# Kernel optimization log

Hardware: AMD Instinct MI355X
Metric: run time of the kernel (lower is better)

## Reference

```python
import jax, jax.numpy as jnp
import numpy as np

NQ = 9  # 9 qubits per 3x3 patch; state shape (M, 2,...,2), axis (NQ-q) holds qubit q (qiskit little-endian)

def _ax(q):
    return NQ - q

def _bcast(theta):
    theta = jnp.asarray(theta)
    if theta.ndim == 1:  # per-patch angle -> broadcast over 8 remaining qubit axes
        return theta.reshape((-1,) + (1,) * (NQ - 1))
    return theta

def apply_1q(state, q, m00, m01, m10, m11):
    ax = _ax(q)
    s0 = jnp.take(state, 0, axis=ax)
    s1 = jnp.take(state, 1, axis=ax)
    return jnp.stack([m00 * s0 + m01 * s1, m10 * s0 + m11 * s1], axis=ax)

def apply_ry(state, q, theta):
    th = _bcast(theta) * 0.5
    c = jnp.cos(th).astype(state.dtype)
    s = jnp.sin(th).astype(state.dtype)
    return apply_1q(state, q, c, -s, s, c)

def apply_rz(state, q, theta):
    th = _bcast(theta) * 0.5
    e = jnp.exp(-1j * th.astype(jnp.complex64))
    return apply_1q(state, q, e, 0.0, 0.0, jnp.conj(e))

def apply_cx(state, c, t):
    axc, axt = _ax(c), _ax(t)
    sc0 = jnp.take(state, 0, axis=axc)
    sc1 = jnp.take(state, 1, axis=axc)
    axt2 = axt - 1 if axt > axc else axt
    sc1 = jnp.flip(sc1, axis=axt2)  # X on target within control=1 subspace
    return jnp.stack([sc0, sc1], axis=axc)

def apply_crx(state, c, t, theta):
    axc, axt = _ax(c), _ax(t)
    sc0 = jnp.take(state, 0, axis=axc)
    sc1 = jnp.take(state, 1, axis=axc)
    axt2 = axt - 1 if axt > axc else axt
    t0 = jnp.take(sc1, 0, axis=axt2)
    t1 = jnp.take(sc1, 1, axis=axt2)
    co = jnp.cos(theta * 0.5)
    si = jnp.sin(theta * 0.5)
    sc1 = jnp.stack([co * t0 - 1j * si * t1, -1j * si * t0 + co * t1], axis=axt2)
    return jnp.stack([sc0, sc1], axis=axc)

def qcnn_batched(angles, w):
    """angles: (M, 9) input rotation angles. w: (42,) shared weights. Returns (M, 3) = [<X>,<Y>,<Z>] on qubit 0."""
    M = angles.shape[0]
    state = jnp.zeros((M,) + (2,) * NQ, dtype=jnp.complex64)
    state = state.at[(slice(None),) + (0,) * NQ].set(1.0)
    for q in range(NQ):  # input encoding
        state = apply_ry(state, q, angles[:, q])
    wi = 0
    # conv1: RY + RZ on all 9 qubits, ring CNOT
    for q in range(NQ):
        state = apply_ry(state, q, w[wi]); wi += 1
    for q in range(NQ):
        state = apply_rz(state, q, w[wi]); wi += 1
    for i in range(NQ):
        state = apply_cx(state, i, (i + 1) % NQ)
    # pool1: 6 CRX gates
    for (c, t) in [(1, 0), (2, 0), (4, 3), (5, 3), (7, 6), (8, 6)]:
        state = apply_crx(state, c, t, w[wi]); wi += 1
    # conv2 on qubits [0,3,6]
    for q in [0, 3, 6]:
        state = apply_ry(state, q, w[wi]); wi += 1
    for q in [0, 3, 6]:
        state = apply_rz(state, q, w[wi]); wi += 1
    for (c, t) in [(0, 3), (3, 6), (6, 0)]:
        state = apply_cx(state, c, t)
    state = apply_ry(state, 0, w[wi])
    state = apply_rz(state, 3, w[wi + 1]); wi += 2
    # pool2
    state = apply_crx(state, 3, 0, w[wi])
    state = apply_crx(state, 3, 6, w[wi + 1])
    state = apply_ry(state, 0, w[wi + 2])
    state = apply_ry(state, 6, w[wi + 3]); wi += 4
    # conv3
    state = apply_ry(state, 0, w[wi])
    state = apply_ry(state, 6, w[wi + 1])
    state = apply_cx(state, 0, 6)
    state = apply_rz(state, 0, w[wi + 2])
    state = apply_rz(state, 6, w[wi + 3]); wi += 4
    # pool3
    state = apply_crx(state, 6, 0, w[wi])
    state = apply_ry(state, 0, w[wi + 1]); wi += 2
    assert wi == 42
    # expectations <X>,<Y>,<Z> on qubit 0 (last axis)
    a0 = jnp.take(state, 0, axis=NQ)
    a1 = jnp.take(state, 1, axis=NQ)
    axes = tuple(range(1, NQ))
    z = jnp.sum(jnp.conj(a0) * a1, axis=axes)
    ex = 2.0 * jnp.real(z)
    ey = 2.0 * jnp.imag(z)
    ez = jnp.sum(jnp.abs(a0) ** 2 - jnp.abs(a1) ** 2, axis=axes)
    return jnp.stack([ex, ey, ez], axis=-1).astype(jnp.float32)

def setup_inputs() -> dict:
    key = jax.random.key(0)
    k1, k2, k3 = jax.random.split(key, 3)
    B, H, WS, NCLS = 8, 28, 3, 10
    n = H - WS + 1  # 26 patches per side
    x = jax.random.uniform(k1, (B, 1, H, H), dtype=jnp.float32)
    w = jax.random.normal(k2, (42,), dtype=jnp.float32)
    fc_w = jax.random.normal(k3, (NCLS, n * n * 3), dtype=jnp.float32) * 0.02
    fc_b = jnp.zeros((NCLS,), dtype=jnp.float32)
    return {"x": x, "w": w, "fc_w": fc_w, "fc_b": fc_b}

def reference(x, w, fc_w, fc_b):
    B, H, WS = x.shape[0], x.shape[2], 3
    n = H - WS + 1
    # extract 3x3 patches, row-major within window (matches torch unfold+view)
    patches = jnp.stack([x[:, 0, i:i + n, j:j + n] for i in range(WS) for j in range(WS)], axis=-1)  # (B,n,n,9)
    angles = patches.reshape(B * n * n, WS * WS) * jnp.pi
    bloch = qcnn_batched(angles, w)  # (B*N, 3)
    feats = bloch.reshape(B, n * n * 3)  # patch-major [X,Y,Z] per patch, matches torch.cat over patches
    return feats @ fc_w.T + fc_b
```

## Files before the change

### kernel.cpp

```cpp
#include <hip/hip_runtime.h>


__device__ __forceinline__ float shx(float v, int m) { return __shfl_xor(v, m, 64); }

__device__ __forceinline__ float2 cmul(float2 a, float2 b) {
  return make_float2(a.x * b.x - a.y * b.y, a.x * b.y + a.y * b.x);
}

template <int TM> __device__ __forceinline__
void ry_r(float (&re)[8], float (&im)[8], float c, float s) {
#pragma unroll
  for (int r0 = 0; r0 < 8; ++r0) if (!(r0 & TM)) {
    const int r1 = r0 | TM;
    float a = re[r0], bb = re[r1];
    re[r0] = c * a - s * bb; re[r1] = s * a + c * bb;
    a = im[r0]; bb = im[r1];
    im[r0] = c * a - s * bb; im[r1] = s * a + c * bb;
  }
}
template <int TM> __device__ __forceinline__
void rz_r(float (&re)[8], float (&im)[8], float c, float s) {
#pragma unroll
  for (int r = 0; r < 8; ++r) {
    const float sg = (r & TM) ? s : -s;
    const float a = re[r], bb = im[r];
    re[r] = c * a - sg * bb;
    im[r] = c * bb + sg * a;
  }
}
template <int CM, int TM> __device__ __forceinline__
void cx_rr(float (&re)[8], float (&im)[8]) {
#pragma unroll
  for (int r0 = 0; r0 < 8; ++r0) if ((r0 & CM) && !(r0 & TM)) {
    const int r1 = r0 | TM;
    float t = re[r0]; re[r0] = re[r1]; re[r1] = t;
    t = im[r0]; im[r0] = im[r1]; im[r1] = t;
  }
}
template <int CM, int TM> __device__ __forceinline__
void crx_rr(float (&re)[8], float (&im)[8], float co, float si) {
#pragma unroll
  for (int r0 = 0; r0 < 8; ++r0) if ((r0 & CM) && !(r0 & TM)) {
    const int r1 = r0 | TM;
    const float r0r = re[r0], r0i = im[r0], r1r = re[r1], r1i = im[r1];
    re[r0] = co * r0r + si * r1i; im[r0] = co * r0i - si * r1r;
    re[r1] = co * r1r + si * r0i; im[r1] = co * r1i - si * r0r;
  }
}

__global__ __launch_bounds__(256) void qcnn_fused(const float* __restrict__ x,
                                                  const float* __restrict__ w,
                                                  float* __restrict__ feats) {
  __shared__ float  wenc[9];
  __shared__ float2 zcs[9];
  __shared__ float2 g[24];
  __shared__ float2 rxtab[3][4];
  __shared__ float4 Msh[8][4];

  const int tid = threadIdx.x;
  if (tid < 9) {
    wenc[tid] = w[tid];
  } else if (tid >= 16 && tid < 25) {
    float s, c; __sincosf(0.5f * w[9 + (tid - 16)], &s, &c);
    zcs[tid - 16] = make_float2(c, s);
  } else if (tid >= 32 && tid < 56) {
    float s, c; __sincosf(0.5f * w[18 + (tid - 32)], &s, &c);
    g[tid - 32] = make_float2(c, s);
  } else if (tid >= 56 && tid < 68) {
    const int k = tid - 56, a = k >> 2, cb = k & 3;
    float th = 0.0f;
    if (cb & 1) th += w[18 + 2 * a];
    if (cb & 2) th += w[19 + 2 * a];
    float s, c; __sincosf(0.5f * th, &s, &c);
    rxtab[a][cb] = make_float2(c, s);
  }
  __syncthreads();

  if (tid < 8) {
    float re[8], im[8];
#pragma unroll
    for (int r = 0; r < 8; ++r) { re[r] = (r == tid) ? 1.0f : 0.0f; im[r] = 0.0f; }
    ry_r<1>(re, im, g[6].x, g[6].y);
    ry_r<2>(re, im, g[7].x, g[7].y);
    ry_r<4>(re, im, g[8].x, g[8].y);
    rz_r<1>(re, im, g[9].x, g[9].y);
    rz_r<2>(re, im, g[10].x, g[10].y);
    rz_r<4>(re, im, g[11].x, g[11].y);
    cx_rr<1, 2>(re, im);
    cx_rr<2, 4>(re, im);
    cx_rr<4, 1>(re, im);
    ry_r<1>(re, im, g[12].x, g[12].y);
    rz_r<2>(re, im, g[13].x, g[13].y);
    crx_rr<2, 1>(re, im, g[14].x, g[14].y);
    crx_rr<2, 4>(re, im, g[15].x, g[15].y);
    ry_r<1>(re, im, g[16].x, g[16].y);
    ry_r<4>(re, im, g[17].x, g[17].y);
    ry_r<1>(re, im, g[18].x, g[18].y);
    ry_r<4>(re, im, g[19].x, g[19].y);
    cx_rr<1, 4>(re, im);
    rz_r<1>(re, im, g[20].x, g[20].y);
    rz_r<4>(re, im, g[21].x, g[21].y);
    crx_rr<4, 1>(re, im, g[22].x, g[22].y);
    ry_r<1>(re, im, g[23].x, g[23].y);
    float* mp = (float*)&Msh[0][0];
#pragma unroll
    for (int i = 0; i < 8; ++i) {
      mp[i * 16 + (tid >> 1) * 4 + 2 * (tid & 1) + 0] = re[i];
      mp[i * 16 + (tid >> 1) * 4 + 2 * (tid & 1) + 1] = im[i];
    }
  }

  const int lane = tid & 63;
  const unsigned p = blockIdx.x * 4u + (tid >> 6);
  const unsigned b = p / 676u;
  const unsigned rem = p - b * 676u;
  const unsigned i = rem / 26u, j = rem - i * 26u;

  float c_enc = 0.0f, s_enc = 0.0f;
  if (lane < 9) {
    const int di = lane / 3, dj = lane - di * 3;
    const float xv = x[b * 784u + (i + di) * 28u + (j + dj)];
    const float ang = fmaf(xv, 3.14159265358979323846f, wenc[lane]) * 0.5f;
    __sincosf(ang, &s_enc, &c_enc);
  }
  float cqv[9], sqv[9];
#pragma unroll
  for (int q = 0; q < 9; ++q) { cqv[q] = __shfl(c_enc, q, 64); sqv[q] = __shfl(s_enc, q, 64); }

  const int l0 = lane & 1, l1 = (lane >> 1) & 1, l2 = (lane >> 2) & 1;
  const int l3 = (lane >> 3) & 1, l4 = (lane >> 4) & 1, l5 = (lane >> 5) & 1;

  auto tau = [&](int bit, int q) -> float2 {
    const float2 z = zcs[q];
    const float m  = bit ? sqv[q] : cqv[q];
    const float zy = bit ? z.y : -z.y;
    return make_float2(m * z.x, m * zy);
  };

  const int a0 = l5, a1 = l0 ^ l5;
  float2 p00 = cmul(tau(a0, 0), tau(a1, 1));
  float2 p01 = cmul(tau(a0 ^ 1, 0), tau(a1 ^ 1, 1));
  float2 p10 = cmul(tau(l1, 3), tau(l2, 4));
  float2 p11 = cmul(tau(l1 ^ 1, 3), tau(l2 ^ 1, 4));
  float2 p20 = cmul(tau(l3, 6), tau(l4, 7));
  float2 p21 = cmul(tau(l3 ^ 1, 6), tau(l4 ^ 1, 7));
  const float2 T = cmul(cmul(tau(l0 ^ l1, 2), tau(l2 ^ l3, 5)), tau(l4 ^ l5, 8));
  p20 = cmul(p20, T);
  p21 = cmul(p21, T);

  {
    const float2 x0 = rxtab[0][lane & 3];
    const float2 x1 = rxtab[1][(lane >> 2) & 3];
    const float2 x2 = rxtab[2][(lane >> 4) & 3];
    float2 nA, nB;
    nA = make_float2(x0.x * p00.x + x0.y * p01.y, x0.x * p00.y - x0.y * p01.x);
    nB = make_float2(x0.x * p01.x + x0.y * p00.y, x0.x * p01.y - x0.y * p00.x);
    p00 = nA; p01 = nB;
    nA = make_float2(x1.x * p10.x + x1.y * p11.y, x1.x * p10.y - x1.y * p11.x);
    nB = make_float2(x1.x * p11.x + x1.y * p10.y, x1.x * p11.y - x1.y * p10.x);
    p10 = nA; p11 = nB;
    nA = make_float2(x2.x * p20.x + x2.y * p21.y, x2.x * p20.y - x2.y * p21.x);
    nB = make_float2(x2.x * p21.x + x2.y * p20.y, x2.x * p21.y - x2.y * p20.x);
    p20 = nA; p21 = nB;
  }

  float ure[8], uim[8];
  {
    const float2 q00 = cmul(p00, p10), q01v = cmul(p01, p10);
    const float2 q10 = cmul(p00, p11), q11v = cmul(p01, p11);
    const float2 qq[4] = {q00, q01v, q10, q11v};
#pragma unroll
    for (int r = 0; r < 8; ++r) {
      const float2 u = cmul(qq[r & 3], (r & 4) ? p21 : p20);
      ure[r] = u.x; uim[r] = u.y;
    }
  }

  __syncthreads();

  float nre[8], nim[8];
#pragma unroll
  for (int oi = 0; oi < 8; ++oi) {
    float ar = 0.0f, ai = 0.0f;
#pragma unroll
    for (int jj = 0; jj < 4; ++jj) {
      const float4 m = Msh[oi][jj];
      ar = fmaf(m.x, ure[2 * jj], ar);     ar = fmaf(-m.y, uim[2 * jj], ar);
      ai = fmaf(m.x, uim[2 * jj], ai);     ai = fmaf(m.y, ure[2 * jj], ai);
      ar = fmaf(m.z, ure[2 * jj + 1], ar); ar = fmaf(-m.w, uim[2 * jj + 1], ar);
      ai = fmaf(m.z, uim[2 * jj + 1], ai); ai = fmaf(m.w, ure[2 * jj + 1], ai);
    }
    nre[oi] = ar; nim[oi] = ai;
  }

  float zr = 0.f, zi = 0.f, pe = 0.f;
#pragma unroll
  for (int r0 = 0; r0 < 8; r0 += 2) {
    const int r1 = r0 + 1;
    zr += nre[r0] * nre[r1] + nim[r0] * nim[r1];
    zi += nre[r0] * nim[r1] - nim[r0] * nre[r1];
    pe += nre[r0] * nre[r0] + nim[r0] * nim[r0];
  }
#pragma unroll
  for (int m = 1; m < 64; m <<= 1) { zr += shx(zr, m); zi += shx(zi, m); pe += shx(pe, m); }

  if (lane == 0) {
    feats[p * 3u + 0u] = 2.0f * zr;
    feats[p * 3u + 1u] = 2.0f * zi;
    feats[p * 3u + 2u] = 2.0f * pe - 1.0f;
  }
}

__global__ __launch_bounds__(256) void fc_kernel(const float* __restrict__ feats,
                                                 const float* __restrict__ fc_w,
                                                 const float* __restrict__ fc_b,
                                                 float* __restrict__ out) {
  const int b = blockIdx.x / 10, c = blockIdx.x - b * 10;
  const float* f = feats + b * 2028;
  const float* wr = fc_w + c * 2028;
  float acc = 0.0f;
  for (int k = threadIdx.x; k < 2028; k += 256) acc += f[k] * wr[k];
#pragma unroll
  for (int m = 1; m < 64; m <<= 1) acc += __shfl_xor(acc, m, 64);
  __shared__ float sbuf[4];
  const int lane = threadIdx.x & 63, wv = threadIdx.x >> 6;
  if (lane == 0) sbuf[wv] = acc;
  __syncthreads();
  if (threadIdx.x == 0) out[b * 10 + c] = sbuf[0] + sbuf[1] + sbuf[2] + sbuf[3] + fc_b[c];
}

extern "C" void kernel_launch(void* const* d_in, const int* in_sizes, int n_in,
                              void* d_out, int out_size, void* d_ws, size_t ws_size,
                              hipStream_t stream) {
  const float* x    = (const float*)d_in[0];
  const float* w    = (const float*)d_in[1];
  const float* fc_w = (const float*)d_in[2];
  const float* fc_b = (const float*)d_in[3];
  float* out = (float*)d_out;

  const int B = in_sizes[0] / 784;
  const int npatch = B * 676;

  float* feats = (float*)d_ws;

  qcnn_fused<<<npatch / 4, 256, 0, stream>>>(x, w, feats);
  fc_kernel<<<B * 10, 256, 0, stream>>>(feats, fc_w, fc_b, out);
}
```

Baseline: 70.50 us.

## Fuse FC into QCNN kernel via last-block counter and drop per-block 8x8 matrix build

Merges the FC reduction into the main kernel: each block atomically increments a global counter, and the last block to finish computes all the FC outputs. The per-block 8x8 unitary construction and its block-wide barrier are removed. Early gates are instead applied as factored single-qubit ops before the tensor product, with the rest applied directly on registers. Trig tables are now computed per wave, so no block-level sync is needed. This trades a second kernel launch for a memset launch plus an atomic, and the FC tail now runs serially in a single block.

```diff
diff --git a/kernel.cpp b/kernel.cpp
--- a/kernel.cpp
+++ b/kernel.cpp
@@ -48,93 +48,77 @@
   }
 }
 
-__global__ __launch_bounds__(256) void qcnn_fused(const float* __restrict__ x,
-                                                  const float* __restrict__ w,
-                                                  float* __restrict__ feats) {
-  __shared__ float  wenc[9];
-  __shared__ float2 zcs[9];
-  __shared__ float2 g[24];
-  __shared__ float2 rxtab[3][4];
-  __shared__ float4 Msh[8][4];
+__device__ __forceinline__
+void ry_f(float2& A, float2& B, float c, float s) {
+  const float2 nA = make_float2(c * A.x - s * B.x, c * A.y - s * B.y);
+  const float2 nB = make_float2(s * A.x + c * B.x, s * A.y + c * B.y);
+  A = nA; B = nB;
+}
+__device__ __forceinline__
+void rz_f(float2& A, float2& B, float c, float s) {
+  A = make_float2(c * A.x + s * A.y, c * A.y - s * A.x);
+  B = make_float2(c * B.x - s * B.y, c * B.y + s * B.x);
+}
+__device__ __forceinline__
+void rx_f(float2& A, float2& B, float c, float s) {
+  const float2 nA = make_float2(c * A.x + s * B.y, c * A.y - s * B.x);
+  const float2 nB = make_float2(c * B.x + s * A.y, c * B.y - s * A.x);
+  A = nA; B = nB;
+}
+
+__global__ __launch_bounds__(256) void qcnn_all(const float* __restrict__ x,
+                                                const float* __restrict__ w,
+                                                const float* __restrict__ fc_w,
+                                                const float* __restrict__ fc_b,
+                                                float* __restrict__ feats,
+                                                unsigned int* __restrict__ counter,
+                                                float* __restrict__ out,
+                                                int nblk) {
+  __shared__ float4 tauT[4][9];
+  __shared__ float2 rxT[4][12];
+  __shared__ float2 gT[4][16];
 
   const int tid = threadIdx.x;
-  if (tid < 9) {
-    wenc[tid] = w[tid];
-  } else if (tid >= 16 && tid < 25) {
-    float s, c; __sincosf(0.5f * w[9 + (tid - 16)], &s, &c);
-    zcs[tid - 16] = make_float2(c, s);
-  } else if (tid >= 32 && tid < 56) {
-    float s, c; __sincosf(0.5f * w[18 + (tid - 32)], &s, &c);
-    g[tid - 32] = make_float2(c, s);
-  } else if (tid >= 56 && tid < 68) {
-    const int k = tid - 56, a = k >> 2, cb = k & 3;
+  const int wv = tid >> 6, lane = tid & 63;
+  const unsigned p = blockIdx.x * 4u + wv;
+  const unsigned b = p / 676u;
+  const unsigned rem = p - b * 676u;
+  const unsigned i = rem / 26u, j = rem - i * 26u;
+
+  if (lane < 9) {
+    const int di = lane / 3, dj = lane - di * 3;
+    const float xv = x[b * 784u + (i + di) * 28u + (j + dj)];
+    const float ang = fmaf(xv, 3.14159265358979323846f, w[lane]) * 0.5f;
+    float s, c; __sincosf(ang, &s, &c);
+    float zs, zc; __sincosf(0.5f * w[9 + lane], &zs, &zc);
+    tauT[wv][lane] = make_float4(c * zc, -c * zs, s * zc, s * zs);
+  } else if (lane < 21) {
+    const int k = lane - 9, a = k >> 2, cb = k & 3;
     float th = 0.0f;
     if (cb & 1) th += w[18 + 2 * a];
     if (cb & 2) th += w[19 + 2 * a];
     float s, c; __sincosf(0.5f * th, &s, &c);
-    rxtab[a][cb] = make_float2(c, s);
-  }
-  __syncthreads();
-
-  if (tid < 8) {
-    float re[8], im[8];
-#pragma unroll
-    for (int r = 0; r < 8; ++r) { re[r] = (r == tid) ? 1.0f : 0.0f; im[r] = 0.0f; }
-    ry_r<1>(re, im, g[6].x, g[6].y);
-    ry_r<2>(re, im, g[7].x, g[7].y);
-    ry_r<4>(re, im, g[8].x, g[8].y);
-    rz_r<1>(re, im, g[9].x, g[9].y);
-    rz_r<2>(re, im, g[10].x, g[10].y);
-    rz_r<4>(re, im, g[11].x, g[11].y);
-    cx_rr<1, 2>(re, im);
-    cx_rr<2, 4>(re, im);
-    cx_rr<4, 1>(re, im);
-    ry_r<1>(re, im, g[12].x, g[12].y);
-    rz_r<2>(re, im, g[13].x, g[13].y);
-    crx_rr<2, 1>(re, im, g[14].x, g[14].y);
-    crx_rr<2, 4>(re, im, g[15].x, g[15].y);
-    ry_r<1>(re, im, g[16].x, g[16].y);
-    ry_r<4>(re, im, g[17].x, g[17].y);
-    ry_r<1>(re, im, g[18].x, g[18].y);
-    ry_r<4>(re, im, g[19].x, g[19].y);
-    cx_rr<1, 4>(re, im);
-    rz_r<1>(re, im, g[20].x, g[20].y);
-    rz_r<4>(re, im, g[21].x, g[21].y);
-    crx_rr<4, 1>(re, im, g[22].x, g[22].y);
-    ry_r<1>(re, im, g[23].x, g[23].y);
-    float* mp = (float*)&Msh[0][0];
-#pragma unroll
-    for (int i = 0; i < 8; ++i) {
-      mp[i * 16 + (tid >> 1) * 4 + 2 * (tid & 1) + 0] = re[i];
-      mp[i * 16 + (tid >> 1) * 4 + 2 * (tid & 1) + 1] = im[i];
-    }
-  }
-
-  const int lane = tid & 63;
-  const unsigned p = blockIdx.x * 4u + (tid >> 6);
-  const unsigned b = p / 676u;
-  const unsigned rem = p - b * 676u;
-  const unsigned i = rem / 26u, j = rem - i * 26u;
-
-  float c_enc = 0.0f, s_enc = 0.0f;
-  if (lane < 9) {
-    const int di = lane / 3, dj = lane - di * 3;
-    const float xv = x[b * 784u + (i + di) * 28u + (j + dj)];
-    const float ang = fmaf(xv, 3.14159265358979323846f, wenc[lane]) * 0.5f;
-    __sincosf(ang, &s_enc, &c_enc);
-  }
-  float cqv[9], sqv[9];
-#pragma unroll
-  for (int q = 0; q < 9; ++q) { cqv[q] = __shfl(c_enc, q, 64); sqv[q] = __shfl(s_enc, q, 64); }
+    rxT[wv][k] = make_float2(c, s);
+  } else if (lane < 37) {
+    const int k = lane - 21;
+    float th;
+    if (k < 10)       th = w[24 + k];
+    else if (k == 10) th = w[34] + w[36];
+    else if (k == 11) th = w[35] + w[37];
+    else              th = w[26 + k];
+    float s, c; __sincosf(0.5f * th, &s, &c);
+    gT[wv][k] = make_float2(c, s);
+  }
 
   const int l0 = lane & 1, l1 = (lane >> 1) & 1, l2 = (lane >> 2) & 1;
   const int l3 = (lane >> 3) & 1, l4 = (lane >> 4) & 1, l5 = (lane >> 5) & 1;
 
+  float4 tq[9];
+#pragma unroll
+  for (int q = 0; q < 9; ++q) tq[q] = tauT[wv][q];
   auto tau = [&](int bit, int q) -> float2 {
-    const float2 z = zcs[q];
-    const float m  = bit ? sqv[q] : cqv[q];
-    const float zy = bit ? z.y : -z.y;
-    return make_float2(m * z.x, m * zy);
+    const float4 t = tq[q];
+    return bit ? make_float2(t.z, t.w) : make_float2(t.x, t.y);
   };
 
   const int a0 = l5, a1 = l0 ^ l5;
@@ -149,22 +133,26 @@
   p21 = cmul(p21, T);
 
   {
-    const float2 x0 = rxtab[0][lane & 3];
-    const float2 x1 = rxtab[1][(lane >> 2) & 3];
-    const float2 x2 = rxtab[2][(lane >> 4) & 3];
-    float2 nA, nB;
-    nA = make_float2(x0.x * p00.x + x0.y * p01.y, x0.x * p00.y - x0.y * p01.x);
-    nB = make_float2(x0.x * p01.x + x0.y * p00.y, x0.x * p01.y - x0.y * p00.x);
-    p00 = nA; p01 = nB;
-    nA = make_float2(x1.x * p10.x + x1.y * p11.y, x1.x * p10.y - x1.y * p11.x);
-    nB = make_float2(x1.x * p11.x + x1.y * p10.y, x1.x * p11.y - x1.y * p10.x);
-    p10 = nA; p11 = nB;
-    nA = make_float2(x2.x * p20.x + x2.y * p21.y, x2.x * p20.y - x2.y * p21.x);
-    nB = make_float2(x2.x * p21.x + x2.y * p20.y, x2.x * p21.y - x2.y * p20.x);
-    p20 = nA; p21 = nB;
-  }
-
-  float ure[8], uim[8];
+    const float2 x0 = rxT[wv][lane & 3];
+    const float2 x1 = rxT[wv][4 + ((lane >> 2) & 3)];
+    const float2 x2 = rxT[wv][8 + ((lane >> 4) & 3)];
+    rx_f(p00, p01, x0.x, x0.y);
+    rx_f(p10, p11, x1.x, x1.y);
+    rx_f(p20, p21, x2.x, x2.y);
+  }
+
+  {
+    const float2 g0 = gT[wv][0], g1 = gT[wv][1], g2 = gT[wv][2];
+    const float2 g3 = gT[wv][3], g4 = gT[wv][4], g5 = gT[wv][5];
+    ry_f(p00, p01, g0.x, g0.y);
+    ry_f(p10, p11, g1.x, g1.y);
+    ry_f(p20, p21, g2.x, g2.y);
+    rz_f(p00, p01, g3.x, g3.y);
+    rz_f(p10, p11, g4.x, g4.y);
+    rz_f(p20, p21, g5.x, g5.y);
+  }
+
+  float re[8], im[8];
   {
     const float2 q00 = cmul(p00, p10), q01v = cmul(p01, p10);
     const float2 q10 = cmul(p00, p11), q11v = cmul(p01, p11);
@@ -172,34 +160,38 @@
 #pragma unroll
     for (int r = 0; r < 8; ++r) {
       const float2 u = cmul(qq[r & 3], (r & 4) ? p21 : p20);
-      ure[r] = u.x; uim[r] = u.y;
+      re[r] = u.x; im[r] = u.y;
     }
   }
 
-  __syncthreads();
-
-  float nre[8], nim[8];
-#pragma unroll
-  for (int oi = 0; oi < 8; ++oi) {
-    float ar = 0.0f, ai = 0.0f;
-#pragma unroll
-    for (int jj = 0; jj < 4; ++jj) {
-      const float4 m = Msh[oi][jj];
-      ar = fmaf(m.x, ure[2 * jj], ar);     ar = fmaf(-m.y, uim[2 * jj], ar);
-      ai = fmaf(m.x, uim[2 * jj], ai);     ai = fmaf(m.y, ure[2 * jj], ai);
-      ar = fmaf(m.z, ure[2 * jj + 1], ar); ar = fmaf(-m.w, uim[2 * jj + 1], ar);
-      ai = fmaf(m.z, uim[2 * jj + 1], ai); ai = fmaf(m.w, ure[2 * jj + 1], ai);
-    }
-    nre[oi] = ar; nim[oi] = ai;
+  {
+    const float2 g6 = gT[wv][6],  g7 = gT[wv][7],  g8 = gT[wv][8];
+    const float2 g9 = gT[wv][9],  gA = gT[wv][10], gB = gT[wv][11];
+    const float2 gC = gT[wv][12], gD = gT[wv][13], gE = gT[wv][14];
+    const float2 gF = gT[wv][15];
+    cx_rr<1, 2>(re, im);
+    cx_rr<2, 4>(re, im);
+    cx_rr<4, 1>(re, im);
+    ry_r<1>(re, im, g6.x, g6.y);
+    rz_r<2>(re, im, g7.x, g7.y);
+    crx_rr<2, 1>(re, im, g8.x, g8.y);
+    crx_rr<2, 4>(re, im, g9.x, g9.y);
+    ry_r<1>(re, im, gA.x, gA.y);
+    ry_r<4>(re, im, gB.x, gB.y);
+    cx_rr<1, 4>(re, im);
+    rz_r<1>(re, im, gC.x, gC.y);
+    rz_r<4>(re, im, gD.x, gD.y);
+    crx_rr<4, 1>(re, im, gE.x, gE.y);
+    ry_r<1>(re, im, gF.x, gF.y);
   }
 
   float zr = 0.f, zi = 0.f, pe = 0.f;
 #pragma unroll
   for (int r0 = 0; r0 < 8; r0 += 2) {
     const int r1 = r0 + 1;
-    zr += nre[r0] * nre[r1] + nim[r0] * nim[r1];
-    zi += nre[r0] * nim[r1] - nim[r0] * nre[r1];
-    pe += nre[r0] * nre[r0] + nim[r0] * nim[r0];
+    zr += re[r0] * re[r1] + im[r0] * im[r1];
+    zi += re[r0] * im[r1] - im[r0] * re[r1];
+    pe += re[r0] * re[r0] + im[r0] * im[r0];
   }
 #pragma unroll
   for (int m = 1; m < 64; m <<= 1) { zr += shx(zr, m); zi += shx(zi, m); pe += shx(pe, m); }
@@ -209,24 +201,26 @@
     feats[p * 3u + 1u] = 2.0f * zi;
     feats[p * 3u + 2u] = 2.0f * pe - 1.0f;
   }
-}
-
-__global__ __launch_bounds__(256) void fc_kernel(const float* __restrict__ feats,
-                                                 const float* __restrict__ fc_w,
-                                                 const float* __restrict__ fc_b,
-                                                 float* __restrict__ out) {
-  const int b = blockIdx.x / 10, c = blockIdx.x - b * 10;
-  const float* f = feats + b * 2028;
-  const float* wr = fc_w + c * 2028;
-  float acc = 0.0f;
-  for (int k = threadIdx.x; k < 2028; k += 256) acc += f[k] * wr[k];
-#pragma unroll
-  for (int m = 1; m < 64; m <<= 1) acc += __shfl_xor(acc, m, 64);
-  __shared__ float sbuf[4];
-  const int lane = threadIdx.x & 63, wv = threadIdx.x >> 6;
-  if (lane == 0) sbuf[wv] = acc;
+
+  __threadfence();
   __syncthreads();
-  if (threadIdx.x == 0) out[b * 10 + c] = sbuf[0] + sbuf[1] + sbuf[2] + sbuf[3] + fc_b[c];
+  __shared__ unsigned int lastFlag;
+  if (tid == 0) lastFlag = (atomicAdd(counter, 1u) == (unsigned)(nblk - 1)) ? 1u : 0u;
+  __syncthreads();
+  if (lastFlag) {
+    __threadfence();
+    const int q0 = wv * 20;
+    for (int q = q0; q < q0 + 20; ++q) {
+      const int bb = q / 10, cc = q - 10 * bb;
+      const float* f = feats + bb * 2028;
+      const float* wr = fc_w + cc * 2028;
+      float acc = 0.0f;
+      for (int k = lane; k < 2028; k += 64) acc += f[k] * wr[k];
+#pragma unroll
+      for (int m = 1; m < 64; m <<= 1) acc += shx(acc, m);
+      if (lane == 0) out[bb * 10 + cc] = acc + fc_b[cc];
+    }
+  }
 }
 
 extern "C" void kernel_launch(void* const* d_in, const int* in_sizes, int n_in,
@@ -240,9 +234,11 @@
 
   const int B = in_sizes[0] / 784;
   const int npatch = B * 676;
+  const int nblk = npatch / 4;
 
   float* feats = (float*)d_ws;
-
-  qcnn_fused<<<npatch / 4, 256, 0, stream>>>(x, w, feats);
-  fc_kernel<<<B * 10, 256, 0, stream>>>(feats, fc_w, fc_b, out);
-}
+  unsigned int* counter = (unsigned int*)((char*)d_ws + (1 << 20));
+
+  hipMemsetAsync(counter, 0, sizeof(unsigned int), stream);
+  qcnn_all<<<nblk, 256, 0, stream>>>(x, w, fc_w, fc_b, feats, counter, out, nblk);
+}
```

Result: slower. 268.9 us (+281.4%).
